# Kernel optimization log

Measured on AMD Instinct MI355X. Metric: run time of the kernel, lower is better.

Reference implementation:

```python
import jax, jax.numpy as jnp
import numpy as np
import math

C, NH, HD, L, P, FFN = 256, 8, 32, 1, 4, 512
H_BEV, W_BEV = 200, 100
NQ, BS, NV = 1000, 4, H_BEV * W_BEV
EPS = 1e-5


def _ln(x, g, b):
    m = x.mean(-1, keepdims=True)
    v = ((x - m) ** 2).mean(-1, keepdims=True)
    return (x - m) / jnp.sqrt(v + EPS) * g + b


def _mha(x, qpos, in_w, in_b, ow, ob):
    # nn.MultiheadAttention self-attention; key_pos = query_pos (shapes match)
    q = x + qpos
    k = x + qpos
    v = x
    wq, wk, wv = jnp.split(in_w, 3, axis=0)
    bq, bk, bv = jnp.split(in_b, 3, axis=0)
    bs, nq, _ = x.shape
    qh = (q @ wq.T + bq).reshape(bs, nq, NH, HD)
    kh = (k @ wk.T + bk).reshape(bs, nq, NH, HD)
    vh = (v @ wv.T + bv).reshape(bs, nq, NH, HD)
    scores = jnp.einsum('bqhd,bkhd->bhqk', qh, kh) / jnp.sqrt(jnp.float32(HD))
    attn = jax.nn.softmax(scores, axis=-1)
    out = jnp.einsum('bhqk,bkhd->bqhd', attn, vh).reshape(bs, nq, C)
    return out @ ow.T + ob


def _msdeform(x, qpos, value, ref, spatial_shapes, so_w, so_b, aw_w, aw_b, vp_w, vp_b, op_w, op_b):
    # Multi-scale deformable attention (single level), bilinear sampling with
    # align_corners=False convention and zero padding, as in the CUDA kernel.
    bs, nq, _ = x.shape
    q = x + qpos
    v = (value @ vp_w.T + vp_b).reshape(bs, NV, NH, HD).transpose(0, 2, 1, 3)  # [bs,nh,nv,hd]
    off = (q @ so_w.T + so_b).reshape(bs, nq, NH, L, P, 2)
    aw = jax.nn.softmax((q @ aw_w.T + aw_b).reshape(bs, nq, NH, L * P), axis=-1)
    aw = aw.reshape(bs, nq, NH, L, P)
    norm = jnp.stack([spatial_shapes[:, 1], spatial_shapes[:, 0]], -1).astype(jnp.float32)  # [L,2] = (W,H)
    loc = ref[:, :, None, :, None, :] + off / norm[None, None, None, :, None, :]  # [bs,nq,nh,L,P,2]
    loc = loc[:, :, :, 0]  # single level -> [bs,nq,nh,P,2]
    awp = aw[:, :, :, 0]   # [bs,nq,nh,P]
    x_im = loc[..., 0] * W_BEV - 0.5
    y_im = loc[..., 1] * H_BEV - 0.5
    x0 = jnp.floor(x_im)
    y0 = jnp.floor(y_im)
    lx = x_im - x0
    ly = y_im - y0
    x0i = x0.astype(jnp.int32)
    y0i = y0.astype(jnp.int32)
    acc = jnp.zeros((bs, NH, nq, P, HD), jnp.float32)
    for dy in (0, 1):
        for dx in (0, 1):
            xi = x0i + dx
            yi = y0i + dy
            w = (lx if dx else 1.0 - lx) * (ly if dy else 1.0 - ly)  # [bs,nq,nh,P]
            ok = ((xi >= 0) & (xi < W_BEV) & (yi >= 0) & (yi < H_BEV)).astype(jnp.float32)
            idx = jnp.clip(yi, 0, H_BEV - 1) * W_BEV + jnp.clip(xi, 0, W_BEV - 1)
            idx_t = idx.transpose(0, 2, 1, 3).reshape(bs, NH, nq * P)
            g = jnp.take_along_axis(v, idx_t[..., None], axis=2).reshape(bs, NH, nq, P, HD)
            acc = acc + g * (w * ok).transpose(0, 2, 1, 3)[..., None]
    out = (acc * awp.transpose(0, 2, 1, 3)[..., None]).sum(3)  # [bs,nh,nq,hd]
    out = out.transpose(0, 2, 1, 3).reshape(bs, nq, C)
    return out @ op_w.T + op_b


def setup_inputs() -> dict:
    key = jax.random.key(0)
    ks = jax.random.split(key, 24)
    f32 = jnp.float32

    def w(k, shp):
        fan = shp[-1]
        return (jax.random.normal(k, shp, f32) * (1.0 / np.sqrt(fan))).astype(f32)

    # sampling_offsets bias per _reset_parameters (radial grid init)
    thetas = np.arange(NH, dtype=np.float32) * (2.0 * math.pi / NH)
    grid = np.stack([np.cos(thetas), np.sin(thetas)], -1)
    grid = grid / np.abs(grid).max(-1, keepdims=True)
    grid = np.tile(grid[:, None, None, :], (1, L, P, 1))
    for i in range(P):
        grid[:, :, i, :] *= i + 1
    so_b = jnp.asarray(grid.reshape(-1), f32)

    return {
        'query': jax.random.normal(ks[0], (NQ, BS, C), f32),
        'value': jax.random.normal(ks[1], (NV, BS, C), f32),
        'query_pos': jax.random.normal(ks[2], (NQ, BS, C), f32),
        'reference_points': jax.random.uniform(ks[3], (BS, NQ, L, 2), f32),
        'spatial_shapes': jnp.array([[H_BEV, W_BEV]], jnp.int32),
        'level_start_index': jnp.zeros((L,), jnp.int32),
        'in_proj_w': w(ks[4], (3 * C, C)),
        'in_proj_b': jnp.zeros((3 * C,), f32),
        'mha_ow': w(ks[5], (C, C)),
        'mha_ob': jnp.zeros((C,), f32),
        'so_w': w(ks[6], (NH * L * P * 2, C)) * 0.01,
        'so_b': so_b,
        'aw_w': w(ks[7], (NH * L * P, C)) * 0.01,
        'aw_b': jnp.zeros((NH * L * P,), f32),
        'vp_w': w(ks[8], (C, C)),
        'vp_b': jnp.zeros((C,), f32),
        'op_w': w(ks[9], (C, C)),
        'op_b': jnp.zeros((C,), f32),
        'ffn_w1': w(ks[10], (FFN, C)),
        'ffn_b1': jnp.zeros((FFN,), f32),
        'ffn_w2': w(ks[11], (C, FFN)),
        'ffn_b2': jnp.zeros((C,), f32),
        'ln1_g': jnp.ones((C,), f32), 'ln1_b': jnp.zeros((C,), f32),
        'ln2_g': jnp.ones((C,), f32), 'ln2_b': jnp.zeros((C,), f32),
        'ln3_g': jnp.ones((C,), f32), 'ln3_b': jnp.zeros((C,), f32),
    }


def reference(query, value, query_pos, reference_points, spatial_shapes, level_start_index,
              in_proj_w, in_proj_b, mha_ow, mha_ob, so_w, so_b, aw_w, aw_b,
              vp_w, vp_b, op_w, op_b, ffn_w1, ffn_b1, ffn_w2, ffn_b2,
              ln1_g, ln1_b, ln2_g, ln2_b, ln3_g, ln3_b):
    # batch_first=False: (seq, bs, C) -> (bs, seq, C)
    x = query.transpose(1, 0, 2)
    val = value.transpose(1, 0, 2)
    qpos = query_pos.transpose(1, 0, 2)
    # self_attn -> norm (residual inside attn wrapper; dropout=0 in eval)
    x = _ln(x + _mha(x, qpos, in_proj_w, in_proj_b, mha_ow, mha_ob), ln1_g, ln1_b)
    # cross_attn (MSDeformAttn) -> norm
    x = _ln(x + _msdeform(x, qpos, val, reference_points, spatial_shapes,
                          so_w, so_b, aw_w, aw_b, vp_w, vp_b, op_w, op_b), ln2_g, ln2_b)
    # ffn -> norm
    h = jax.nn.relu(x @ ffn_w1.T + ffn_b1) @ ffn_w2.T + ffn_b2
    x = _ln(x + h, ln3_g, ln3_b)
    return x.transpose(1, 0, 2)
```

## Files before the change

kernel.cpp:

```cpp
#include <hip/hip_runtime.h>
#include <hip/hip_bf16.h>
#include <cmath>

#define BS   4
#define NQ   1000
#define CDIM 256
#define NH   8
#define HD   32
#define NVAL 20000
#define FFND 512
#define PN   4
#define WBEV 100
#define HBEV 200
#define TK   32

typedef __bf16 v8bf __attribute__((ext_vector_type(8)));
typedef float  v4f  __attribute__((ext_vector_type(4)));

__device__ __forceinline__ void gload_lds16(const void* g, void* l) {
    __builtin_amdgcn_global_load_lds(
        (const __attribute__((address_space(1))) unsigned int*)g,
        (__attribute__((address_space(3))) unsigned int*)l, 16, 0, 0);
}

__global__ __launch_bounds__(256) void prep_all_kernel(
    const float* __restrict__ query, const float* __restrict__ qpos,
    const float* __restrict__ in_w, const float* __restrict__ mha_ow,
    const float* __restrict__ vp_w, const float* __restrict__ op_w,
    const float* __restrict__ ffn_w1, const float* __restrict__ ffn_w2,
    const float* __restrict__ so_w, const float* __restrict__ aw_w,
    const float* __restrict__ so_b, const float* __restrict__ aw_b,
    float* __restrict__ x, float* __restrict__ qpos_t,
    __bf16* __restrict__ x_bf, __bf16* __restrict__ xq_bf,
    __bf16* __restrict__ wb, __bf16* __restrict__ wsmall,
    float* __restrict__ bsmall)
{
    int blk = blockIdx.x, tid = threadIdx.x;
    if (blk < 640) {
        long e = ((long)blk * 256 + tid) * 4;
        const float* src; long off;
        if      (e < 196608) { src = in_w;   off = e; }
        else if (e < 262144) { src = mha_ow; off = e - 196608; }
        else if (e < 327680) { src = vp_w;   off = e - 262144; }
        else if (e < 393216) { src = op_w;   off = e - 327680; }
        else if (e < 524288) { src = ffn_w1; off = e - 393216; }
        else                 { src = ffn_w2; off = e - 524288; }
        float4 v = *(const float4*)(src + off);
        __bf16* d = wb + e;
        d[0] = (__bf16)v.x; d[1] = (__bf16)v.y; d[2] = (__bf16)v.z; d[3] = (__bf16)v.w;
    } else if (blk < 4640) {
        int qb = blk - 640;
        int q = qb / BS, b = qb % BS;
        float qv = query[(q * BS + b) * CDIM + tid];
        float pv = qpos [(q * BS + b) * CDIM + tid];
        int o = (b * NQ + q) * CDIM + tid;
        x[o] = qv; qpos_t[o] = pv;
        x_bf[o] = (__bf16)qv; xq_bf[o] = (__bf16)(qv + pv);
    } else if (blk < 4672) {
        long e = ((long)(blk - 4640) * 256 + tid) * 4;
        int row = (int)(e >> 8), col = (int)(e & 255);
        float4 v = {0.f, 0.f, 0.f, 0.f};
        if (row < 64)      v = *(const float4*)(so_w + row * 256 + col);
        else if (row < 96) v = *(const float4*)(aw_w + (row - 64) * 256 + col);
        __bf16* d = wsmall + e;
        d[0] = (__bf16)v.x; d[1] = (__bf16)v.y; d[2] = (__bf16)v.z; d[3] = (__bf16)v.w;
    } else {
        if (tid < 128) bsmall[tid] = tid < 64 ? so_b[tid] : (tid < 96 ? aw_b[tid - 64] : 0.f);
    }
}

template<int TBM, int TBN>
__global__ __launch_bounds__(256) void mgemm_kernel(
    const __bf16* __restrict__ A, const __bf16* __restrict__ W,
    const float* __restrict__ bias, float* __restrict__ Yf,
    __bf16* __restrict__ Yb, int M, int N, int K, int relu)
{
    constexpr int WMF = TBM / 32;
    constexpr int WNF = TBN / 32;
    __shared__ __bf16 As[TBM][64];
    __shared__ __bf16 Bs[TBN][64];
    int bm = blockIdx.y * TBM, bn = blockIdx.x * TBN;
    int tid = threadIdx.x;
    int wave = tid >> 6, lane = tid & 63, quad = lane >> 4, n16 = lane & 15;
    int wm = (wave & 1) * (TBM / 2), wn = (wave >> 1) * (TBN / 2);
    v4f acc[WMF][WNF] = {};

    for (int k0 = 0; k0 < K; k0 += 64) {
        __syncthreads();
        #pragma unroll
        for (int i = 0; i < TBM * 8 / 256; i++) {
            int e = i * 256 + tid;
            int r = e >> 3, c = (e & 7) ^ (r & 7);
            int row = bm + r; if (row > M - 1) row = M - 1;
            gload_lds16(A + (long)row * K + k0 + c * 8, &As[0][0] + e * 8);
        }
        #pragma unroll
        for (int i = 0; i < TBN * 8 / 256; i++) {
            int e = i * 256 + tid;
            int r = e >> 3, c = (e & 7) ^ (r & 7);
            gload_lds16(W + (long)(bn + r) * K + k0 + c * 8, &Bs[0][0] + e * 8);
        }
        __syncthreads();
        #pragma unroll
        for (int s = 0; s < 2; s++) {
            v8bf af[WMF], bfr[WNF];
            #pragma unroll
            for (int mi = 0; mi < WMF; mi++) {
                int row = wm + mi * 16 + n16;
                af[mi] = *(v8bf*)&As[row][(((quad + s * 4) ^ (row & 7))) * 8];
            }
            #pragma unroll
            for (int nj = 0; nj < WNF; nj++) {
                int row = wn + nj * 16 + n16;
                bfr[nj] = *(v8bf*)&Bs[row][(((quad + s * 4) ^ (row & 7))) * 8];
            }
            #pragma unroll
            for (int mi = 0; mi < WMF; mi++)
                #pragma unroll
                for (int nj = 0; nj < WNF; nj++)
                    acc[mi][nj] = __builtin_amdgcn_mfma_f32_16x16x32_bf16(af[mi], bfr[nj], acc[mi][nj], 0, 0, 0);
        }
    }

    #pragma unroll
    for (int mi = 0; mi < WMF; mi++) {
        #pragma unroll
        for (int r = 0; r < 4; r++) {
            int m = bm + wm + mi * 16 + quad * 4 + r;
            if (m >= M) continue;
            #pragma unroll
            for (int nj = 0; nj < WNF; nj++) {
                int nn = bn + wn + nj * 16 + n16;
                if (nn >= N) continue;
                float v = acc[mi][nj][r] + bias[nn];
                if (relu) v = fmaxf(v, 0.f);
                if (Yf) Yf[(long)m * N + nn] = v;
                if (Yb) Yb[(long)m * N + nn] = (__bf16)v;
            }
        }
    }
}

__global__ __launch_bounds__(256) void qkv_kernel(
    const __bf16* __restrict__ xq, const __bf16* __restrict__ xv,
    const __bf16* __restrict__ W, const float* __restrict__ bias,
    __bf16* __restrict__ qk, __bf16* __restrict__ vh)
{
    __shared__ __bf16 As[64][64];
    __shared__ __bf16 Bs[64][64];
    int bm = blockIdx.y * 64, bn = blockIdx.x * 64;
    const __bf16* A = (bn < 512) ? xq : xv;
    int tid = threadIdx.x;
    int wave = tid >> 6, lane = tid & 63, quad = lane >> 4, n16 = lane & 15;
    int wm = (wave & 1) * 32, wn = (wave >> 1) * 32;
    v4f acc[2][2] = {};

    for (int k0 = 0; k0 < 256; k0 += 64) {
        __syncthreads();
        #pragma unroll
        for (int i = 0; i < 2; i++) {
            int e = i * 256 + tid;
            int r = e >> 3, c = (e & 7) ^ (r & 7);
            int row = bm + r; if (row > BS * NQ - 1) row = BS * NQ - 1;
            gload_lds16(A + (long)row * 256 + k0 + c * 8, &As[0][0] + e * 8);
        }
        #pragma unroll
        for (int i = 0; i < 2; i++) {
            int e = i * 256 + tid;
            int r = e >> 3, c = (e & 7) ^ (r & 7);
            gload_lds16(W + (long)(bn + r) * 256 + k0 + c * 8, &Bs[0][0] + e * 8);
        }
        __syncthreads();
        #pragma unroll
        for (int s = 0; s < 2; s++) {
            v8bf af[2], bfr[2];
            #pragma unroll
            for (int mi = 0; mi < 2; mi++) {
                int row = wm + mi * 16 + n16;
                af[mi] = *(v8bf*)&As[row][(((quad + s * 4) ^ (row & 7))) * 8];
            }
            #pragma unroll
            for (int nj = 0; nj < 2; nj++) {
                int row = wn + nj * 16 + n16;
                bfr[nj] = *(v8bf*)&Bs[row][(((quad + s * 4) ^ (row & 7))) * 8];
            }
            #pragma unroll
            for (int mi = 0; mi < 2; mi++)
                #pragma unroll
                for (int nj = 0; nj < 2; nj++)
                    acc[mi][nj] = __builtin_amdgcn_mfma_f32_16x16x32_bf16(af[mi], bfr[nj], acc[mi][nj], 0, 0, 0);
        }
    }

    #pragma unroll
    for (int mi = 0; mi < 2; mi++) {
        #pragma unroll
        for (int r = 0; r < 4; r++) {
            int m = bm + wm + mi * 16 + quad * 4 + r;
            if (m >= BS * NQ) continue;
            #pragma unroll
            for (int nj = 0; nj < 2; nj++) {
                int nn = bn + wn + nj * 16 + n16;
                float v = acc[mi][nj][r] + bias[nn];
                if (nn < 512) qk[(long)m * 512 + nn] = (__bf16)v;
                else          vh[(long)m * 256 + (nn - 512)] = (__bf16)v;
            }
        }
    }
}

template<int KD, int MODE>
__global__ __launch_bounds__(256) void gemmln_kernel(
    const __bf16* __restrict__ A, const __bf16* __restrict__ W,
    const float* __restrict__ bias, const float* __restrict__ res,
    const float* __restrict__ g, const float* __restrict__ beta,
    const float* __restrict__ qpos_t,
    float* __restrict__ outf, __bf16* __restrict__ outb)
{
    __shared__ __bf16 As[16][64];
    __shared__ __bf16 Bs[256][64];
    __shared__ float redS[4][16], redQ[4][16];
    int bm = blockIdx.x * 16;
    int tid = threadIdx.x;
    int wave = tid >> 6, lane = tid & 63, quad = lane >> 4, n16 = lane & 15;
    int wn = wave * 64;
    v4f acc[4] = {};

    for (int k0 = 0; k0 < KD; k0 += 64) {
        __syncthreads();
        if (tid < 128) {
            int e = tid;
            int r = e >> 3, c = (e & 7) ^ (r & 7);
            gload_lds16(A + (long)(bm + r) * KD + k0 + c * 8, &As[0][0] + e * 8);
        }
        #pragma unroll
        for (int i = 0; i < 8; i++) {
            int e = i * 256 + tid;
            int r = e >> 3, c = (e & 7) ^ (r & 7);
            gload_lds16(W + (long)r * KD + k0 + c * 8, &Bs[0][0] + e * 8);
        }
        __syncthreads();
        #pragma unroll
        for (int s = 0; s < 2; s++) {
            v8bf af = *(v8bf*)&As[n16][(((quad + s * 4) ^ (n16 & 7))) * 8];
            #pragma unroll
            for (int nj = 0; nj < 4; nj++) {
                int row = wn + nj * 16 + n16;
                v8bf bfr = *(v8bf*)&Bs[row][(((quad + s * 4) ^ (row & 7))) * 8];
                acc[nj] = __builtin_amdgcn_mfma_f32_16x16x32_bf16(af, bfr, acc[nj], 0, 0, 0);
            }
        }
    }

    float y[4][4], s1[4] = {}, s2[4] = {};
    #pragma unroll
    for (int r = 0; r < 4; r++) {
        int m = bm + quad * 4 + r;
        #pragma unroll
        for (int nj = 0; nj < 4; nj++) {
            int nn = wn + nj * 16 + n16;
            float v = acc[nj][r] + bias[nn] + res[(long)m * 256 + nn];
            y[r][nj] = v;
            s1[r] += v; s2[r] += v * v;
        }
    }
    #pragma unroll
    for (int r = 0; r < 4; r++) {
        #pragma unroll
        for (int off = 1; off < 16; off <<= 1) {
            s1[r] += __shfl_xor(s1[r], off, 16);
            s2[r] += __shfl_xor(s2[r], off, 16);
        }
    }
    if (n16 == 0) {
        #pragma unroll
        for (int r = 0; r < 4; r++) {
            redS[wave][quad * 4 + r] = s1[r];
            redQ[wave][quad * 4 + r] = s2[r];
        }
    }
    __syncthreads();
    #pragma unroll
    for (int r = 0; r < 4; r++) {
        int mr = quad * 4 + r;
        float ts = redS[0][mr] + redS[1][mr] + redS[2][mr] + redS[3][mr];
        float tq = redQ[0][mr] + redQ[1][mr] + redQ[2][mr] + redQ[3][mr];
        float mean = ts * (1.0f / 256.0f);
        float var = tq * (1.0f / 256.0f) - mean * mean;
        float rinv = rsqrtf(var + 1e-5f);
        int m = bm + mr;
        #pragma unroll
        for (int nj = 0; nj < 4; nj++) {
            int nn = wn + nj * 16 + n16;
            float o = (y[r][nj] - mean) * rinv * g[nn] + beta[nn];
            if (MODE == 0) {
                outf[(long)m * 256 + nn] = o;
                outb[(long)m * 256 + nn] = (__bf16)(o + qpos_t[(long)m * 256 + nn]);
            } else if (MODE == 1) {
                outf[(long)m * 256 + nn] = o;
                outb[(long)m * 256 + nn] = (__bf16)o;
            } else {
                int b = m / NQ, q = m % NQ;
                outf[(long)(q * BS + b) * 256 + nn] = o;
            }
        }
    }
}

__global__ __launch_bounds__(256) void vgemm_kernel(
    const float* __restrict__ A, const __bf16* __restrict__ W,
    const float* __restrict__ bias, __bf16* __restrict__ Yb)
{
    constexpr int WMF = 4, WNF = 4;
    __shared__ __bf16 As[128][64];
    __shared__ __bf16 Bs[128][64];
    int bm = blockIdx.y * 128, bn = blockIdx.x * 128;
    int tid = threadIdx.x;
    int wave = tid >> 6, lane = tid & 63, quad = lane >> 4, n16 = lane & 15;
    int wm = (wave & 1) * 64, wn = (wave >> 1) * 64;
    v4f acc[WMF][WNF] = {};

    for (int k0 = 0; k0 < 256; k0 += 64) {
        float4 fa[4][2];
        #pragma unroll
        for (int i = 0; i < 4; i++) {
            int e = i * 256 + tid;
            int r = e >> 3, c = (e & 7) ^ (r & 7);
            const float* p = A + (long)(bm + r) * 256 + k0 + c * 8;
            fa[i][0] = *(const float4*)p;
            fa[i][1] = *(const float4*)(p + 4);
        }
        __syncthreads();
        #pragma unroll
        for (int i = 0; i < 4; i++) {
            int e = i * 256 + tid;
            v8bf v;
            v[0] = (__bf16)fa[i][0].x; v[1] = (__bf16)fa[i][0].y;
            v[2] = (__bf16)fa[i][0].z; v[3] = (__bf16)fa[i][0].w;
            v[4] = (__bf16)fa[i][1].x; v[5] = (__bf16)fa[i][1].y;
            v[6] = (__bf16)fa[i][1].z; v[7] = (__bf16)fa[i][1].w;
            *(v8bf*)(&As[0][0] + e * 8) = v;
        }
        #pragma unroll
        for (int i = 0; i < 4; i++) {
            int e = i * 256 + tid;
            int r = e >> 3, c = (e & 7) ^ (r & 7);
            gload_lds16(W + (long)(bn + r) * 256 + k0 + c * 8, &Bs[0][0] + e * 8);
        }
        __syncthreads();
        #pragma unroll
        for (int s = 0; s < 2; s++) {
            v8bf af[WMF], bfr[WNF];
            #pragma unroll
            for (int mi = 0; mi < WMF; mi++) {
                int row = wm + mi * 16 + n16;
                af[mi] = *(v8bf*)&As[row][(((quad + s * 4) ^ (row & 7))) * 8];
            }
            #pragma unroll
            for (int nj = 0; nj < WNF; nj++) {
                int row = wn + nj * 16 + n16;
                bfr[nj] = *(v8bf*)&Bs[row][(((quad + s * 4) ^ (row & 7))) * 8];
            }
            #pragma unroll
            for (int mi = 0; mi < WMF; mi++)
                #pragma unroll
                for (int nj = 0; nj < WNF; nj++)
                    acc[mi][nj] = __builtin_amdgcn_mfma_f32_16x16x32_bf16(af[mi], bfr[nj], acc[mi][nj], 0, 0, 0);
        }
    }

    #pragma unroll
    for (int mi = 0; mi < WMF; mi++) {
        #pragma unroll
        for (int r = 0; r < 4; r++) {
            int m = bm + wm + mi * 16 + quad * 4 + r;
            #pragma unroll
            for (int nj = 0; nj < WNF; nj++) {
                int nn = bn + wn + nj * 16 + n16;
                Yb[(long)m * 256 + nn] = (__bf16)(acc[mi][nj][r] + bias[nn]);
            }
        }
    }
}

__global__ __launch_bounds__(256) void fattn_kernel(
    const __bf16* __restrict__ qk, const __bf16* __restrict__ vh,
    __bf16* __restrict__ out)
{
    __shared__ __bf16 Ks[2][TK][40];
    __shared__ __bf16 Vt[2][HD][40];
    __shared__ __bf16 Pl[4][16][40];
    int qt = blockIdx.x, h = blockIdx.y, b = blockIdx.z;
    int tid = threadIdx.x;
    int wave = tid >> 6, lane = tid & 63;
    int quad = lane >> 4, n = lane & 15;
    int q0 = qt * 64 + wave * 16;
    const float scale = 0.17677669529663687f;
    const float M0 = 8.0f;

    int qrow = q0 + n; if (qrow > NQ - 1) qrow = NQ - 1;
    v8bf aq = *(const v8bf*)(qk + (long)(b * NQ + qrow) * 512 + h * HD + quad * 8);

    v4f o0 = {}, o1 = {};
    float lp[4] = {0.f, 0.f, 0.f, 0.f};

    int sv = tid >> 7;
    int t2 = tid & 127;
    int key = t2 >> 2;
    int d8 = (t2 & 3) * 8;
    int vcol = key ^ (((d8 >> 3) & 1) << 4);

    auto loadtile = [&](int k0) -> v8bf {
        int krow = k0 + key; if (krow > NQ - 1) krow = NQ - 1;
        const __bf16* p = sv ? (vh + (long)(b * NQ + krow) * CDIM + h * HD + d8)
                             : (qk + (long)(b * NQ + krow) * 512 + 256 + h * HD + d8);
        return *(const v8bf*)p;
    };

    v8bf stg = loadtile(0);
    int pb = 0;
    for (int k0 = 0; k0 < NQ; k0 += TK) {
        if (sv == 0) {
            *(v8bf*)&Ks[pb][key][d8] = stg;
        } else {
            #pragma unroll
            for (int j = 0; j < 8; j++) Vt[pb][d8 + j][vcol] = stg[j];
        }
        if (k0 + TK < NQ) stg = loadtile(k0 + TK);
        __syncthreads();

        v8bf bk0 = *(v8bf*)&Ks[pb][n][quad * 8];
        v8bf bk1 = *(v8bf*)&Ks[pb][16 + n][quad * 8];
        v4f z = {};
        v4f S0 = __builtin_amdgcn_mfma_f32_16x16x32_bf16(aq, bk0, z, 0, 0, 0);
        v4f S1 = __builtin_amdgcn_mfma_f32_16x16x32_bf16(aq, bk1, z, 0, 0, 0);

        bool last = (k0 + TK > NQ);
        float p0[4], p1[4];
        #pragma unroll
        for (int r = 0; r < 4; r++) {
            p0[r] = __expf(fmaf(S0[r], scale, -M0));
            p1[r] = __expf(fmaf(S1[r], scale, -M0));
            if (last) {
                if (k0 + n >= NQ)      p0[r] = 0.f;
                if (k0 + 16 + n >= NQ) p1[r] = 0.f;
            }
            lp[r] += p0[r] + p1[r];
        }
        #pragma unroll
        for (int r = 0; r < 4; r++) {
            Pl[wave][quad * 4 + r][n]      = (__bf16)p0[r];
            Pl[wave][quad * 4 + r][16 + n] = (__bf16)p1[r];
        }
        asm volatile("s_waitcnt lgkmcnt(0)" ::: "memory");
        v8bf ap = *(v8bf*)&Pl[wave][n][quad * 8];
        int vc = (quad * 8) ^ (((n >> 3) & 1) << 4);
        v8bf bv0 = *(v8bf*)&Vt[pb][n][vc];
        v8bf bv1 = *(v8bf*)&Vt[pb][16 + n][vc];
        o0 = __builtin_amdgcn_mfma_f32_16x16x32_bf16(ap, bv0, o0, 0, 0, 0);
        o1 = __builtin_amdgcn_mfma_f32_16x16x32_bf16(ap, bv1, o1, 0, 0, 0);
        pb ^= 1;
    }

    #pragma unroll
    for (int r = 0; r < 4; r++) {
        float l = lp[r];
        #pragma unroll
        for (int off = 1; off < 16; off <<= 1) l += __shfl_xor(l, off, 16);
        int q = q0 + quad * 4 + r;
        if (q < NQ) {
            float invl = 1.0f / l;
            __bf16* op = out + ((long)(b * NQ + q) * CDIM + h * HD);
            op[n]      = (__bf16)(o0[r] * invl);
            op[16 + n] = (__bf16)(o1[r] * invl);
        }
    }
}

__global__ __launch_bounds__(256) void msds_kernel(
    const __bf16* __restrict__ vproj, const float* __restrict__ soaw,
    const float* __restrict__ refp, __bf16* __restrict__ out)
{
    int bq = blockIdx.x; int b = bq / NQ; int q = bq % NQ;
    int t = threadIdx.x; int h = t / HD; int d = t % HD;
    float rx = refp[(b * NQ + q) * 2 + 0];
    float ry = refp[(b * NQ + q) * 2 + 1];
    const float* rowp = soaw + (long)(b * NQ + q) * 96;
    const float* offp = rowp + h * 8;
    const float* awp  = rowp + 64 + h * 4;
    float a0 = awp[0], a1 = awp[1], a2 = awp[2], a3 = awp[3];
    float m = fmaxf(fmaxf(a0, a1), fmaxf(a2, a3));
    float e0 = __expf(a0 - m), e1 = __expf(a1 - m), e2 = __expf(a2 - m), e3 = __expf(a3 - m);
    float invs = 1.0f / (e0 + e1 + e2 + e3);
    float acc = 0.f;
    #pragma unroll
    for (int p = 0; p < PN; p++) {
        float ew = (p == 0 ? e0 : p == 1 ? e1 : p == 2 ? e2 : e3) * invs;
        float xim = rx * (float)WBEV + offp[p * 2 + 0] - 0.5f;
        float yim = ry * (float)HBEV + offp[p * 2 + 1] - 0.5f;
        float x0f = floorf(xim), y0f = floorf(yim);
        float lx = xim - x0f, ly = yim - y0f;
        int x0 = (int)x0f, y0 = (int)y0f;
        float gsum = 0.f;
        #pragma unroll
        for (int dy = 0; dy < 2; dy++) {
            #pragma unroll
            for (int dx = 0; dx < 2; dx++) {
                int xi = x0 + dx, yi = y0 + dy;
                float w = (dx ? lx : 1.f - lx) * (dy ? ly : 1.f - ly);
                bool ok = (xi >= 0 && xi < WBEV && yi >= 0 && yi < HBEV);
                int xc = min(max(xi, 0), WBEV - 1);
                int yc = min(max(yi, 0), HBEV - 1);
                int idx = yc * WBEV + xc;
                float gv = (float)vproj[((long)(idx * BS + b)) * CDIM + h * HD + d];
                gsum += (ok ? w : 0.f) * gv;
            }
        }
        acc += ew * gsum;
    }
    out[(b * NQ + q) * CDIM + h * HD + d] = (__bf16)acc;
}

extern "C" void kernel_launch(void* const* d_in, const int* in_sizes, int n_in,
                              void* d_out, int out_size, void* d_ws, size_t ws_size,
                              hipStream_t stream) {
    const float* query = (const float*)d_in[0];
    const float* value = (const float*)d_in[1];
    const float* qpos  = (const float*)d_in[2];
    const float* refp  = (const float*)d_in[3];
    const float* in_w  = (const float*)d_in[6];
    const float* in_b  = (const float*)d_in[7];
    const float* mha_ow = (const float*)d_in[8];
    const float* mha_ob = (const float*)d_in[9];
    const float* so_w  = (const float*)d_in[10];
    const float* so_b  = (const float*)d_in[11];
    const float* aw_w  = (const float*)d_in[12];
    const float* aw_b  = (const float*)d_in[13];
    const float* vp_w  = (const float*)d_in[14];
    const float* vp_b  = (const float*)d_in[15];
    const float* op_w  = (const float*)d_in[16];
    const float* op_b  = (const float*)d_in[17];
    const float* ffn_w1 = (const float*)d_in[18];
    const float* ffn_b1 = (const float*)d_in[19];
    const float* ffn_w2 = (const float*)d_in[20];
    const float* ffn_b2 = (const float*)d_in[21];
    const float* ln1_g = (const float*)d_in[22];
    const float* ln1_b = (const float*)d_in[23];
    const float* ln2_g = (const float*)d_in[24];
    const float* ln2_b = (const float*)d_in[25];
    const float* ln3_g = (const float*)d_in[26];
    const float* ln3_b = (const float*)d_in[27];
    float* out = (float*)d_out;

    const long NTOK = (long)BS * NQ * CDIM;

    float* x      = (float*)d_ws;
    float* qpos_t = x + NTOK;
    float* x1     = qpos_t + NTOK;
    float* x2     = x1 + NTOK;
    float* soaw   = x2 + NTOK;
    float* bsmall = soaw + (long)BS * NQ * 96;
    __bf16* x_bf   = (__bf16*)(bsmall + 128);
    __bf16* xq_bf  = x_bf + NTOK;
    __bf16* qk_bf  = xq_bf + NTOK;
    __bf16* vh_bf  = qk_bf + 2 * NTOK;
    __bf16* aA_bf  = vh_bf + NTOK;
    __bf16* x2_bf  = aA_bf + NTOK;
    __bf16* h1_bf  = x2_bf + NTOK;
    __bf16* vpj_bf = h1_bf + 2 * NTOK;
    __bf16* wb     = vpj_bf + (long)BS * NVAL * CDIM;
    __bf16* inw_b  = wb;
    __bf16* mow_b  = wb + 196608;
    __bf16* vpw_b  = wb + 262144;
    __bf16* opw_b  = wb + 327680;
    __bf16* fw1_b  = wb + 393216;
    __bf16* fw2_b  = wb + 524288;
    __bf16* wsmall = wb + 655360;

    const int M = BS * NQ;
    dim3 blk(256);

    prep_all_kernel<<<4673, blk, 0, stream>>>(
        query, qpos, in_w, mha_ow, vp_w, op_w, ffn_w1, ffn_w2,
        so_w, aw_w, so_b, aw_b,
        x, qpos_t, x_bf, xq_bf, wb, wsmall, bsmall);

    qkv_kernel<<<dim3(12, 63), blk, 0, stream>>>(xq_bf, x_bf, inw_b, in_b, qk_bf, vh_bf);

    fattn_kernel<<<dim3((NQ + 63) / 64, NH, BS), blk, 0, stream>>>(qk_bf, vh_bf, aA_bf);

    gemmln_kernel<256, 0><<<250, blk, 0, stream>>>(
        aA_bf, mow_b, mha_ob, x, ln1_g, ln1_b, qpos_t, x1, xq_bf);

    mgemm_kernel<32, 128><<<dim3(1, 125), blk, 0, stream>>>(
        xq_bf, wsmall, bsmall, soaw, nullptr, M, 96, 256, 0);

    vgemm_kernel<<<dim3(2, 625), blk, 0, stream>>>(value, vpw_b, vp_b, vpj_bf);

    msds_kernel<<<M, blk, 0, stream>>>(vpj_bf, soaw, refp, aA_bf);

    gemmln_kernel<256, 1><<<250, blk, 0, stream>>>(
        aA_bf, opw_b, op_b, x1, ln2_g, ln2_b, nullptr, x2, x2_bf);

    mgemm_kernel<64, 64><<<dim3(8, 63), blk, 0, stream>>>(
        x2_bf, fw1_b, ffn_b1, nullptr, h1_bf, M, 512, 256, 1);

    gemmln_kernel<512, 2><<<250, blk, 0, stream>>>(
        h1_bf, fw2_b, ffn_b2, x2, ln3_g, ln3_b, nullptr, out, nullptr);
}
```

Baseline: 279.9 us.

## Merge value-projection GEMM and self-attention into one heterogeneous launch

```diff
diff --git a/kernel.cpp b/kernel.cpp
--- a/kernel.cpp
+++ b/kernel.cpp
@@ -307,172 +307,182 @@
     }
 }
 
-__global__ __launch_bounds__(256) void vgemm_kernel(
-    const float* __restrict__ A, const __bf16* __restrict__ W,
-    const float* __restrict__ bias, __bf16* __restrict__ Yb)
+__global__ __launch_bounds__(256) void fvg_kernel(
+    const float* __restrict__ value, const __bf16* __restrict__ Wv,
+    const float* __restrict__ bv, __bf16* __restrict__ vpj,
+    const __bf16* __restrict__ qk, const __bf16* __restrict__ vh,
+    __bf16* __restrict__ aout)
 {
-    constexpr int WMF = 4, WNF = 4;
-    __shared__ __bf16 As[128][64];
-    __shared__ __bf16 Bs[128][64];
-    int bm = blockIdx.y * 128, bn = blockIdx.x * 128;
+    __shared__ __align__(16) char smem[32768];
     int tid = threadIdx.x;
     int wave = tid >> 6, lane = tid & 63, quad = lane >> 4, n16 = lane & 15;
-    int wm = (wave & 1) * 64, wn = (wave >> 1) * 64;
-    v4f acc[WMF][WNF] = {};
-
-    for (int k0 = 0; k0 < 256; k0 += 64) {
+
+    if (blockIdx.x < 1250) {
+        int vb = blockIdx.x;
+        int bm = (vb >> 1) * 128, bn = (vb & 1) * 128;
+        __bf16* As = (__bf16*)smem;
+        __bf16* Bs = (__bf16*)(smem + 16384);
+        int wm = (wave & 1) * 64, wn = (wave >> 1) * 64;
+        v4f acc[4][4] = {};
         float4 fa[4][2];
+
         #pragma unroll
         for (int i = 0; i < 4; i++) {
             int e = i * 256 + tid;
             int r = e >> 3, c = (e & 7) ^ (r & 7);
-            const float* p = A + (long)(bm + r) * 256 + k0 + c * 8;
+            const float* p = value + (long)(bm + r) * 256 + c * 8;
             fa[i][0] = *(const float4*)p;
             fa[i][1] = *(const float4*)(p + 4);
         }
-        __syncthreads();
-        #pragma unroll
-        for (int i = 0; i < 4; i++) {
-            int e = i * 256 + tid;
-            v8bf v;
-            v[0] = (__bf16)fa[i][0].x; v[1] = (__bf16)fa[i][0].y;
-            v[2] = (__bf16)fa[i][0].z; v[3] = (__bf16)fa[i][0].w;
-            v[4] = (__bf16)fa[i][1].x; v[5] = (__bf16)fa[i][1].y;
-            v[6] = (__bf16)fa[i][1].z; v[7] = (__bf16)fa[i][1].w;
-            *(v8bf*)(&As[0][0] + e * 8) = v;
-        }
-        #pragma unroll
-        for (int i = 0; i < 4; i++) {
-            int e = i * 256 + tid;
-            int r = e >> 3, c = (e & 7) ^ (r & 7);
-            gload_lds16(W + (long)(bn + r) * 256 + k0 + c * 8, &Bs[0][0] + e * 8);
-        }
-        __syncthreads();
-        #pragma unroll
-        for (int s = 0; s < 2; s++) {
-            v8bf af[WMF], bfr[WNF];
-            #pragma unroll
-            for (int mi = 0; mi < WMF; mi++) {
-                int row = wm + mi * 16 + n16;
-                af[mi] = *(v8bf*)&As[row][(((quad + s * 4) ^ (row & 7))) * 8];
-            }
-            #pragma unroll
-            for (int nj = 0; nj < WNF; nj++) {
-                int row = wn + nj * 16 + n16;
-                bfr[nj] = *(v8bf*)&Bs[row][(((quad + s * 4) ^ (row & 7))) * 8];
-            }
-            #pragma unroll
-            for (int mi = 0; mi < WMF; mi++)
-                #pragma unroll
-                for (int nj = 0; nj < WNF; nj++)
-                    acc[mi][nj] = __builtin_amdgcn_mfma_f32_16x16x32_bf16(af[mi], bfr[nj], acc[mi][nj], 0, 0, 0);
-        }
-    }
-
-    #pragma unroll
-    for (int mi = 0; mi < WMF; mi++) {
+        for (int s4 = 0; s4 < 4; s4++) {
+            int k0 = s4 * 64;
+            __syncthreads();
+            #pragma unroll
+            for (int i = 0; i < 4; i++) {
+                int e = i * 256 + tid;
+                v8bf v;
+                v[0] = (__bf16)fa[i][0].x; v[1] = (__bf16)fa[i][0].y;
+                v[2] = (__bf16)fa[i][0].z; v[3] = (__bf16)fa[i][0].w;
+                v[4] = (__bf16)fa[i][1].x; v[5] = (__bf16)fa[i][1].y;
+                v[6] = (__bf16)fa[i][1].z; v[7] = (__bf16)fa[i][1].w;
+                *(v8bf*)(As + e * 8) = v;
+            }
+            #pragma unroll
+            for (int i = 0; i < 4; i++) {
+                int e = i * 256 + tid;
+                int r = e >> 3, c = (e & 7) ^ (r & 7);
+                gload_lds16(Wv + (long)(bn + r) * 256 + k0 + c * 8, Bs + e * 8);
+            }
+            __syncthreads();
+            if (s4 < 3) {
+                #pragma unroll
+                for (int i = 0; i < 4; i++) {
+                    int e = i * 256 + tid;
+                    int r = e >> 3, c = (e & 7) ^ (r & 7);
+                    const float* p = value + (long)(bm + r) * 256 + k0 + 64 + c * 8;
+                    fa[i][0] = *(const float4*)p;
+                    fa[i][1] = *(const float4*)(p + 4);
+                }
+            }
+            #pragma unroll
+            for (int s = 0; s < 2; s++) {
+                v8bf af[4], bfr[4];
+                #pragma unroll
+                for (int mi = 0; mi < 4; mi++) {
+                    int row = wm + mi * 16 + n16;
+                    af[mi] = *(v8bf*)&As[row * 64 + (((quad + s * 4) ^ (row & 7))) * 8];
+                }
+                #pragma unroll
+                for (int nj = 0; nj < 4; nj++) {
+                    int row = wn + nj * 16 + n16;
+                    bfr[nj] = *(v8bf*)&Bs[row * 64 + (((quad + s * 4) ^ (row & 7))) * 8];
+                }
+                #pragma unroll
+                for (int mi = 0; mi < 4; mi++)
+                    #pragma unroll
+                    for (int nj = 0; nj < 4; nj++)
+                        acc[mi][nj] = __builtin_amdgcn_mfma_f32_16x16x32_bf16(af[mi], bfr[nj], acc[mi][nj], 0, 0, 0);
+            }
+        }
+        #pragma unroll
+        for (int mi = 0; mi < 4; mi++) {
+            #pragma unroll
+            for (int r = 0; r < 4; r++) {
+                int m = bm + wm + mi * 16 + quad * 4 + r;
+                #pragma unroll
+                for (int nj = 0; nj < 4; nj++) {
+                    int nn = bn + wn + nj * 16 + n16;
+                    vpj[(long)m * 256 + nn] = (__bf16)(acc[mi][nj][r] + bv[nn]);
+                }
+            }
+        }
+    } else {
+        int fb = blockIdx.x - 1250;
+        int qt = fb & 15, h = (fb >> 4) & 7, b = fb >> 7;
+        __bf16* Ks = (__bf16*)smem;
+        __bf16* Vt = (__bf16*)(smem + 5120);
+        __bf16* Pl = (__bf16*)(smem + 10240);
+        int n = n16;
+        int q0 = qt * 64 + wave * 16;
+        const float scale = 0.17677669529663687f;
+        const float M0 = 8.0f;
+
+        int qrow = q0 + n; if (qrow > NQ - 1) qrow = NQ - 1;
+        v8bf aq = *(const v8bf*)(qk + (long)(b * NQ + qrow) * 512 + h * HD + quad * 8);
+
+        v4f o0 = {}, o1 = {};
+        float lp[4] = {0.f, 0.f, 0.f, 0.f};
+
+        int sv = tid >> 7;
+        int t2 = tid & 127;
+        int key = t2 >> 2;
+        int d8 = (t2 & 3) * 8;
+        int vcol = key ^ (((d8 >> 3) & 1) << 4);
+
+        auto loadtile = [&](int k0) -> v8bf {
+            int krow = k0 + key; if (krow > NQ - 1) krow = NQ - 1;
+            const __bf16* p = sv ? (vh + (long)(b * NQ + krow) * CDIM + h * HD + d8)
+                                 : (qk + (long)(b * NQ + krow) * 512 + 256 + h * HD + d8);
+            return *(const v8bf*)p;
+        };
+
+        v8bf stg = loadtile(0);
+        int pb = 0;
+        for (int k0 = 0; k0 < NQ; k0 += TK) {
+            if (sv == 0) {
+                *(v8bf*)&Ks[(pb * TK + key) * 40 + d8] = stg;
+            } else {
+                #pragma unroll
+                for (int j = 0; j < 8; j++) Vt[(pb * HD + d8 + j) * 40 + vcol] = stg[j];
+            }
+            if (k0 + TK < NQ) stg = loadtile(k0 + TK);
+            __syncthreads();
+
+            v8bf bk0 = *(v8bf*)&Ks[(pb * TK + n) * 40 + quad * 8];
+            v8bf bk1 = *(v8bf*)&Ks[(pb * TK + 16 + n) * 40 + quad * 8];
+            v4f z = {};
+            v4f S0 = __builtin_amdgcn_mfma_f32_16x16x32_bf16(aq, bk0, z, 0, 0, 0);
+            v4f S1 = __builtin_amdgcn_mfma_f32_16x16x32_bf16(aq, bk1, z, 0, 0, 0);
+
+            bool last = (k0 + TK > NQ);
+            float p0[4], p1[4];
+            #pragma unroll
+            for (int r = 0; r < 4; r++) {
+                p0[r] = __expf(fmaf(S0[r], scale, -M0));
+                p1[r] = __expf(fmaf(S1[r], scale, -M0));
+                if (last) {
+                    if (k0 + n >= NQ)      p0[r] = 0.f;
+                    if (k0 + 16 + n >= NQ) p1[r] = 0.f;
+                }
+                lp[r] += p0[r] + p1[r];
+            }
+            #pragma unroll
+            for (int r = 0; r < 4; r++) {
+                Pl[(wave * 16 + quad * 4 + r) * 40 + n]      = (__bf16)p0[r];
+                Pl[(wave * 16 + quad * 4 + r) * 40 + 16 + n] = (__bf16)p1[r];
+            }
+            asm volatile("s_waitcnt lgkmcnt(0)" ::: "memory");
+            v8bf ap = *(v8bf*)&Pl[(wave * 16 + n) * 40 + quad * 8];
+            int vc = (quad * 8) ^ (((n >> 3) & 1) << 4);
+            v8bf bv0 = *(v8bf*)&Vt[(pb * HD + n) * 40 + vc];
+            v8bf bv1 = *(v8bf*)&Vt[(pb * HD + 16 + n) * 40 + vc];
+            o0 = __builtin_amdgcn_mfma_f32_16x16x32_bf16(ap, bv0, o0, 0, 0, 0);
+            o1 = __builtin_amdgcn_mfma_f32_16x16x32_bf16(ap, bv1, o1, 0, 0, 0);
+            pb ^= 1;
+        }
+
         #pragma unroll
         for (int r = 0; r < 4; r++) {
-            int m = bm + wm + mi * 16 + quad * 4 + r;
-            #pragma unroll
-            for (int nj = 0; nj < WNF; nj++) {
-                int nn = bn + wn + nj * 16 + n16;
-                Yb[(long)m * 256 + nn] = (__bf16)(acc[mi][nj][r] + bias[nn]);
-            }
-        }
-    }
-}
-
-__global__ __launch_bounds__(256) void fattn_kernel(
-    const __bf16* __restrict__ qk, const __bf16* __restrict__ vh,
-    __bf16* __restrict__ out)
-{
-    __shared__ __bf16 Ks[2][TK][40];
-    __shared__ __bf16 Vt[2][HD][40];
-    __shared__ __bf16 Pl[4][16][40];
-    int qt = blockIdx.x, h = blockIdx.y, b = blockIdx.z;
-    int tid = threadIdx.x;
-    int wave = tid >> 6, lane = tid & 63;
-    int quad = lane >> 4, n = lane & 15;
-    int q0 = qt * 64 + wave * 16;
-    const float scale = 0.17677669529663687f;
-    const float M0 = 8.0f;
-
-    int qrow = q0 + n; if (qrow > NQ - 1) qrow = NQ - 1;
-    v8bf aq = *(const v8bf*)(qk + (long)(b * NQ + qrow) * 512 + h * HD + quad * 8);
-
-    v4f o0 = {}, o1 = {};
-    float lp[4] = {0.f, 0.f, 0.f, 0.f};
-
-    int sv = tid >> 7;
-    int t2 = tid & 127;
-    int key = t2 >> 2;
-    int d8 = (t2 & 3) * 8;
-    int vcol = key ^ (((d8 >> 3) & 1) << 4);
-
-    auto loadtile = [&](int k0) -> v8bf {
-        int krow = k0 + key; if (krow > NQ - 1) krow = NQ - 1;
-        const __bf16* p = sv ? (vh + (long)(b * NQ + krow) * CDIM + h * HD + d8)
-                             : (qk + (long)(b * NQ + krow) * 512 + 256 + h * HD + d8);
-        return *(const v8bf*)p;
-    };
-
-    v8bf stg = loadtile(0);
-    int pb = 0;
-    for (int k0 = 0; k0 < NQ; k0 += TK) {
-        if (sv == 0) {
-            *(v8bf*)&Ks[pb][key][d8] = stg;
-        } else {
-            #pragma unroll
-            for (int j = 0; j < 8; j++) Vt[pb][d8 + j][vcol] = stg[j];
-        }
-        if (k0 + TK < NQ) stg = loadtile(k0 + TK);
-        __syncthreads();
-
-        v8bf bk0 = *(v8bf*)&Ks[pb][n][quad * 8];
-        v8bf bk1 = *(v8bf*)&Ks[pb][16 + n][quad * 8];
-        v4f z = {};
-        v4f S0 = __builtin_amdgcn_mfma_f32_16x16x32_bf16(aq, bk0, z, 0, 0, 0);
-        v4f S1 = __builtin_amdgcn_mfma_f32_16x16x32_bf16(aq, bk1, z, 0, 0, 0);
-
-        bool last = (k0 + TK > NQ);
-        float p0[4], p1[4];
-        #pragma unroll
-        for (int r = 0; r < 4; r++) {
-            p0[r] = __expf(fmaf(S0[r], scale, -M0));
-            p1[r] = __expf(fmaf(S1[r], scale, -M0));
-            if (last) {
-                if (k0 + n >= NQ)      p0[r] = 0.f;
-                if (k0 + 16 + n >= NQ) p1[r] = 0.f;
-            }
-            lp[r] += p0[r] + p1[r];
-        }
-        #pragma unroll
-        for (int r = 0; r < 4; r++) {
-            Pl[wave][quad * 4 + r][n]      = (__bf16)p0[r];
-            Pl[wave][quad * 4 + r][16 + n] = (__bf16)p1[r];
-        }
-        asm volatile("s_waitcnt lgkmcnt(0)" ::: "memory");
-        v8bf ap = *(v8bf*)&Pl[wave][n][quad * 8];
-        int vc = (quad * 8) ^ (((n >> 3) & 1) << 4);
-        v8bf bv0 = *(v8bf*)&Vt[pb][n][vc];
-        v8bf bv1 = *(v8bf*)&Vt[pb][16 + n][vc];
-        o0 = __builtin_amdgcn_mfma_f32_16x16x32_bf16(ap, bv0, o0, 0, 0, 0);
-        o1 = __builtin_amdgcn_mfma_f32_16x16x32_bf16(ap, bv1, o1, 0, 0, 0);
-        pb ^= 1;
-    }
-
-    #pragma unroll
-    for (int r = 0; r < 4; r++) {
-        float l = lp[r];
-        #pragma unroll
-        for (int off = 1; off < 16; off <<= 1) l += __shfl_xor(l, off, 16);
-        int q = q0 + quad * 4 + r;
-        if (q < NQ) {
-            float invl = 1.0f / l;
-            __bf16* op = out + ((long)(b * NQ + q) * CDIM + h * HD);
-            op[n]      = (__bf16)(o0[r] * invl);
-            op[16 + n] = (__bf16)(o1[r] * invl);
+            float l = lp[r];
+            #pragma unroll
+            for (int off = 1; off < 16; off <<= 1) l += __shfl_xor(l, off, 16);
+            int q = q0 + quad * 4 + r;
+            if (q < NQ) {
+                float invl = 1.0f / l;
+                __bf16* op = aout + ((long)(b * NQ + q) * CDIM + h * HD);
+                op[n]      = (__bf16)(o0[r] * invl);
+                op[16 + n] = (__bf16)(o1[r] * invl);
+            }
         }
     }
 }
@@ -587,7 +597,8 @@
 
     qkv_kernel<<<dim3(12, 63), blk, 0, stream>>>(xq_bf, x_bf, inw_b, in_b, qk_bf, vh_bf);
 
-    fattn_kernel<<<dim3((NQ + 63) / 64, NH, BS), blk, 0, stream>>>(qk_bf, vh_bf, aA_bf);
+    fvg_kernel<<<1762, blk, 0, stream>>>(value, vpw_b, vp_b, vpj_bf,
+                                         qk_bf, vh_bf, aA_bf);
 
     gemmln_kernel<256, 0><<<250, blk, 0, stream>>>(
         aA_bf, mow_b, mha_ob, x, ln1_g, ln1_b, qpos_t, x1, xq_bf);
@@ -595,8 +606,6 @@
     mgemm_kernel<32, 128><<<dim3(1, 125), blk, 0, stream>>>(
         xq_bf, wsmall, bsmall, soaw, nullptr, M, 96, 256, 0);
 
-    vgemm_kernel<<<dim3(2, 625), blk, 0, stream>>>(value, vpw_b, vp_b, vpj_bf);
-
     msds_kernel<<<M, blk, 0, stream>>>(vpj_bf, soaw, refp, aA_bf);
 
     gemmln_kernel<256, 1><<<250, blk, 0, stream>>>(
```

Result: no change. 283.7 us (+1.4%).
